# Performance work log

Hardware: AMD Instinct MI355X
Metric: run time of the kernel (lower is better)

The kernel has to match this reference:

```python
import jax, jax.numpy as jnp
import numpy as np

POOL = (2, 2)
STRIDES = (2, 2)


def setup_inputs() -> dict:
    key = jax.random.key(0)
    k1, k2 = jax.random.split(key)
    B, H, W, C = 32, 64, 64, 128
    oH, oW = H * STRIDES[0], W * STRIDES[1]  # SAME padding
    updates = jax.random.normal(k1, (B, H, W, C), dtype=jnp.float32)
    mask = jax.random.randint(k2, (B, H, W, C), 0, oH * oW * C, dtype=jnp.int32)
    return {"updates": updates, "mask": mask}


def reference(updates, mask):
    B, H, W, C = updates.shape
    oH, oW, oC = H * STRIDES[0], W * STRIDES[1], C  # SAME padding output shape
    m = mask.astype(jnp.int32)
    # Decode flat per-batch index into (y, x); feature/batch come from position.
    y = m // (oW * oC)                      # [B,H,W,C]
    x = (m // oC) % oW                      # [B,H,W,C]
    b = jnp.arange(B, dtype=jnp.int32)[:, None, None, None]  # broadcasts over H,W,C
    f = jnp.arange(oC, dtype=jnp.int32)                      # broadcasts over last dim
    out = jnp.zeros((B, oH, oW, oC), dtype=updates.dtype)
    # tf.scatter_nd sums duplicate indices -> use .add for identical semantics
    return out.at[b, y, x, f].add(updates)
```

## Files before the change

kernel.cpp:

```cpp
#include <hip/hip_runtime.h>


#define HWC (64 * 64 * 128)
#define PBINS 4096
#define NPASS 4

__global__ __launch_bounds__(1024) void unpool_c8(
    const float* __restrict__ upd, const int* __restrict__ mask,
    float* __restrict__ out)
{
    extern __shared__ float acc[];

    int bid = blockIdx.x;
    int b   = bid & 31;
    int c0  = (bid >> 5) << 3;

    int t    = threadIdx.x;
    int q    = t & 1;
    int prow = t >> 1;

    const float* ubase = upd  + (size_t)b * HWC + c0 + q * 4;
    const int*   mbase = mask + (size_t)b * HWC + c0 + q * 4;
    float*       obase = out + ((size_t)b << 21) + c0;

    float4 u[8];
    uint2  pk[8];
    #pragma unroll
    for (int k = 0; k < 8; ++k) {
        int pos = prow + (k << 9);
        u[k] = *(const float4*)(ubase + (size_t)pos * 128);
        int4 m4 = *(const int4*)(mbase + (size_t)pos * 128);
        unsigned b0 = ((unsigned)m4.x) >> 7;
        unsigned b1 = ((unsigned)m4.y) >> 7;
        unsigned b2 = ((unsigned)m4.z) >> 7;
        unsigned b3 = ((unsigned)m4.w) >> 7;
        pk[k].x = b0 | (b1 << 16);
        pk[k].y = b2 | (b3 << 16);
    }

    float4* a4 = (float4*)acc;

    int cbase = q << 2;

    for (int p = 0; p < NPASS; ++p) {
        #pragma unroll
        for (int k = 0; k < 8; ++k)
            a4[t + k * 1024] = make_float4(0.f, 0.f, 0.f, 0.f);
        __syncthreads();

        unsigned up = (unsigned)p;
        #pragma unroll
        for (int k = 0; k < 8; ++k) {
            unsigned b0 = pk[k].x & 0xffffu;
            unsigned b1 = pk[k].x >> 16;
            unsigned b2 = pk[k].y & 0xffffu;
            unsigned b3 = pk[k].y >> 16;
            if ((b0 >> 12) == up) atomicAdd(&acc[((b0 & 4095u) << 3) + cbase + 0], u[k].x);
            if ((b1 >> 12) == up) atomicAdd(&acc[((b1 & 4095u) << 3) + cbase + 1], u[k].y);
            if ((b2 >> 12) == up) atomicAdd(&acc[((b2 & 4095u) << 3) + cbase + 2], u[k].z);
            if ((b3 >> 12) == up) atomicAdd(&acc[((b3 & 4095u) << 3) + cbase + 3], u[k].w);
        }
        __syncthreads();

        #pragma unroll
        for (int k = 0; k < 8; ++k) {
            int idx = t + k * 1024;
            int bin = idx >> 1;
            int qd  = idx & 1;
            *(float4*)(obase + (size_t)(p * PBINS + bin) * 128 + qd * 4) = a4[idx];
        }
        if (p < NPASS - 1) __syncthreads();
    }
}

extern "C" void kernel_launch(void* const* d_in, const int* in_sizes, int n_in,
                              void* d_out, int out_size, void* d_ws, size_t ws_size,
                              hipStream_t stream) {
    const float* upd  = (const float*)d_in[0];
    const int*   mask = (const int*)d_in[1];
    float*       out  = (float*)d_out;

    static bool lds_ok = false;
    if (!lds_ok) {
        hipFuncSetAttribute((const void*)unpool_c8,
                            hipFuncAttributeMaxDynamicSharedMemorySize,
                            PBINS * 8 * 4);
        lds_ok = true;
    }

    unpool_c8<<<512, 1024, PBINS * 8 * 4, stream>>>(upd, mask, out);
}
```

Baseline: 444.0 us.

## Double-buffer LDS accumulator across smaller passes and use lightweight barriers

Splits each block's output into 16 passes of 1024 bins instead of 4 passes of 4096, and alternates between two LDS buffers. The barrier after the store phase goes away, so global stores of one pass can overlap zeroing and atomics of the next. Barriers become an explicit lgkmcnt wait plus s_barrier, so they no longer wait on outstanding global stores. The cost is four times as many passes over the register-held updates (more predicate checks) and more barrier rounds.

```diff
diff --git a/kernel.cpp b/kernel.cpp
--- a/kernel.cpp
+++ b/kernel.cpp
@@ -2,10 +2,15 @@
 
 
 #define HWC (64 * 64 * 128)
-#define PBINS 4096
-#define NPASS 4
+#define PBINS 1024
+#define NPASS 16
 
-__global__ __launch_bounds__(1024) void unpool_c8(
+#define LGKM_BAR() do { \
+    __asm__ __volatile__("s_waitcnt lgkmcnt(0)" ::: "memory"); \
+    __builtin_amdgcn_s_barrier(); \
+} while (0)
+
+__global__ __launch_bounds__(1024) void unpool_db(
     const float* __restrict__ upd, const int* __restrict__ mask,
     float* __restrict__ out)
 {
@@ -38,15 +43,15 @@
         pk[k].y = b2 | (b3 << 16);
     }
 
-    float4* a4 = (float4*)acc;
-
     int cbase = q << 2;
 
     for (int p = 0; p < NPASS; ++p) {
-        #pragma unroll
-        for (int k = 0; k < 8; ++k)
-            a4[t + k * 1024] = make_float4(0.f, 0.f, 0.f, 0.f);
-        __syncthreads();
+        float*  A  = acc + ((p & 1) << 13);
+        float4* a4 = (float4*)A;
+
+        a4[t]        = make_float4(0.f, 0.f, 0.f, 0.f);
+        a4[t + 1024] = make_float4(0.f, 0.f, 0.f, 0.f);
+        LGKM_BAR();
 
         unsigned up = (unsigned)p;
         #pragma unroll
@@ -55,21 +60,20 @@
             unsigned b1 = pk[k].x >> 16;
             unsigned b2 = pk[k].y & 0xffffu;
             unsigned b3 = pk[k].y >> 16;
-            if ((b0 >> 12) == up) atomicAdd(&acc[((b0 & 4095u) << 3) + cbase + 0], u[k].x);
-            if ((b1 >> 12) == up) atomicAdd(&acc[((b1 & 4095u) << 3) + cbase + 1], u[k].y);
-            if ((b2 >> 12) == up) atomicAdd(&acc[((b2 & 4095u) << 3) + cbase + 2], u[k].z);
-            if ((b3 >> 12) == up) atomicAdd(&acc[((b3 & 4095u) << 3) + cbase + 3], u[k].w);
+            if ((b0 >> 10) == up) atomicAdd(&A[((b0 & 1023u) << 3) + cbase + 0], u[k].x);
+            if ((b1 >> 10) == up) atomicAdd(&A[((b1 & 1023u) << 3) + cbase + 1], u[k].y);
+            if ((b2 >> 10) == up) atomicAdd(&A[((b2 & 1023u) << 3) + cbase + 2], u[k].z);
+            if ((b3 >> 10) == up) atomicAdd(&A[((b3 & 1023u) << 3) + cbase + 3], u[k].w);
         }
-        __syncthreads();
+        LGKM_BAR();
 
         #pragma unroll
-        for (int k = 0; k < 8; ++k) {
-            int idx = t + k * 1024;
+        for (int k = 0; k < 2; ++k) {
+            int idx = t + (k << 10);
             int bin = idx >> 1;
             int qd  = idx & 1;
             *(float4*)(obase + (size_t)(p * PBINS + bin) * 128 + qd * 4) = a4[idx];
         }
-        if (p < NPASS - 1) __syncthreads();
     }
 }
 
@@ -82,11 +86,11 @@
 
     static bool lds_ok = false;
     if (!lds_ok) {
-        hipFuncSetAttribute((const void*)unpool_c8,
+        hipFuncSetAttribute((const void*)unpool_db,
                             hipFuncAttributeMaxDynamicSharedMemorySize,
-                            PBINS * 8 * 4);
+                            2 * PBINS * 8 * 4);
         lds_ok = true;
     }
 
-    unpool_c8<<<512, 1024, PBINS * 8 * 4, stream>>>(upd, mask, out);
+    unpool_db<<<512, 1024, 2 * PBINS * 8 * 4, stream>>>(upd, mask, out);
 }
```

New measurement: 437.9 us. About the same (-1.4%).
